# Optimization experiments

Measured on AMD Instinct MI355X. Metric: run time of the kernel, lower is better.

## Reference

```python
import jax, jax.numpy as jnp
import numpy as np

S, D_IN, D = 4, 1024, 256   # n_scales, input dim, d_per_scale (d_model=1024)
B, T = 4, 4096
R_MIN, R_MAX, TH_MIN, TH_MAX = 0.9, 0.999, 0.01, 1.0


def setup_inputs() -> dict:
    key = jax.random.key(0)
    ks = jax.random.split(key, 6)
    s_in = 1.0 / np.sqrt(D_IN)
    s_h = 1.0 / np.sqrt(D)
    return {
        'x':   jax.random.normal(ks[0], (B, T, D_IN), jnp.float32),
        'Wg1': jax.random.normal(ks[1], (S, D_IN, D), jnp.float32) * s_in,
        'bg1': jnp.zeros((S, D), jnp.float32),
        'Wg2': jax.random.normal(ks[2], (S, D, D), jnp.float32) * s_h,
        'bg2': jnp.full((S, D), -4.0, jnp.float32),  # bias_init=constant(-4.0)
        'Wdr': jax.random.normal(ks[3], (S, D_IN, D), jnp.float32) * s_in,
        'bdr': jnp.zeros((S, D), jnp.float32),
        'Wdi': jax.random.normal(ks[4], (S, D_IN, D), jnp.float32) * s_in,
        'bdi': jnp.zeros((S, D), jnp.float32),
    }


def _scale_consts():
    r = np.concatenate([[1.0], np.linspace(R_MAX, R_MIN, S - 1)])
    theta = np.concatenate([[0.0], np.linspace(TH_MIN, TH_MAX, S - 1)])
    a_base = (r * np.exp(1j * theta)).astype(np.complex64)        # (S,)
    bscale = np.where(r >= 1.0, 1.0 / np.sqrt(D), 1.0 - r).astype(np.float32)  # (S,)
    return jnp.asarray(a_base), jnp.asarray(bscale)


def reference(x, Wg1, bg1, Wg2, bg2, Wdr, bdr, Wdi, bdi):
    a_base, bscale = _scale_consts()
    # gate MLP (conditioning = x): (B,S,T,D)
    g1 = jax.nn.relu(jnp.einsum('bti,sid->bstd', x, Wg1) + bg1[None, :, None, :])
    gate = jax.nn.sigmoid(jnp.einsum('bstd,sde->bste', g1, Wg2) + bg2[None, :, None, :])
    # complex drive
    dre = jnp.einsum('bti,sid->bstd', x, Wdr) + bdr[None, :, None, :]
    dim = jnp.einsum('bti,sid->bstd', x, Wdi) + bdi[None, :, None, :]
    omg = (1.0 - gate).astype(jnp.complex64)                       # (B,S,T,D)
    a = omg * a_base[None, :, None, None]
    b = omg * ((dre + 1j * dim).astype(jnp.complex64) * bscale[None, :, None, None])
    # linear recurrence h_t = a_t*h_{t-1} + b_t via associative scan along time
    def binop(left, right):
        al, bl = left
        ar, br = right
        return (al * ar, ar * bl + br)
    _, h = jax.lax.associative_scan(binop, (a, b), axis=2)         # (B,S,T,D)
    h = jnp.moveaxis(h, 1, 2)                                      # (B,T,S,D)
    out = jnp.stack([h.real, h.imag], axis=3)                      # (B,T,S,2,D) -> re/im per scale
    return out.reshape(B, T, S * 2 * D)
```

## Files before the change

### kernel.cpp

```cpp
#include <hip/hip_runtime.h>
#include <cmath>

#define S_   4
#define DIN  1024
#define D_   256
#define B_   4
#define T_   4096
#define BT_  (B_*T_)
#define GN   (S_*3*D_)
#define CHUNKS 128
#define CL   (T_/CHUNKS)

typedef short bf16x8 __attribute__((ext_vector_type(8)));
typedef float f32x4  __attribute__((ext_vector_type(4)));

struct SC { float are[S_]; float aim[S_]; float bsc[S_]; };

__device__ inline unsigned short f2bf(float f) {
    unsigned int u = __builtin_bit_cast(unsigned int, f);
    unsigned int r = (u + 0x7FFFu + ((u >> 16) & 1u)) >> 16;
    return (unsigned short)r;
}
__device__ inline float bf2f_lo(unsigned int u) {
    return __builtin_bit_cast(float, u << 16);
}
__device__ inline float bf2f_hi(unsigned int u) {
    return __builtin_bit_cast(float, u & 0xFFFF0000u);
}
__device__ inline float u16om(unsigned int u) {
    return ((float)u + 0.5f) * (1.f/65536.f);
}

#define GLD_LDS(gp, lp) \
    __builtin_amdgcn_global_load_lds( \
        (const __attribute__((address_space(1))) void*)(gp), \
        (__attribute__((address_space(3))) void*)(lp), 16, 0, 0)

__global__ __launch_bounds__(256) void kconv_x(
    const float* __restrict__ x, unsigned short* __restrict__ xb)
{
    const size_t i = ((size_t)blockIdx.x*256 + threadIdx.x)*4;
    const float4 v = *(const float4*)(x + i);
    ushort4 o;
    o.x = f2bf(v.x); o.y = f2bf(v.y); o.z = f2bf(v.z); o.w = f2bf(v.w);
    *(ushort4*)(xb + i) = o;
}

__global__ __launch_bounds__(256) void kconv_w(
    const float* __restrict__ src, unsigned short* __restrict__ dst,
    int K, int N, size_t dst_s_stride)
{
    __shared__ float t[32][33];
    const int k0 = blockIdx.x*32, n0 = blockIdx.y*32, s = blockIdx.z;
    const float* sp = src + (size_t)s*K*N;
    unsigned short* dp = dst + (size_t)s*dst_s_stride;
    const int c = threadIdx.x & 31, r0 = threadIdx.x >> 5;
    #pragma unroll
    for (int p = 0; p < 4; ++p)
        t[r0 + p*8][c] = sp[(size_t)(k0 + r0 + p*8)*N + n0 + c];
    __syncthreads();
    #pragma unroll
    for (int p = 0; p < 4; ++p)
        dp[(size_t)(n0 + r0 + p*8)*K + k0 + c] = f2bf(t[c][r0 + p*8]);
}

__global__ __launch_bounds__(256) void kconv_w3(
    const float* __restrict__ Wg1, const float* __restrict__ Wdr,
    const float* __restrict__ Wdi, unsigned short* __restrict__ dst)
{
    __shared__ float t[32][33];
    const int z = blockIdx.z;
    const int widx = z >> 2, s = z & 3;
    const float* src = (widx == 0) ? Wg1 : ((widx == 1) ? Wdr : Wdi);
    const float* sp = src + (size_t)s*DIN*D_;
    unsigned short* dp = dst + (size_t)s*768*DIN + (size_t)widx*D_*DIN;
    const int k0 = blockIdx.x*32, n0 = blockIdx.y*32;
    const int c = threadIdx.x & 31, r0 = threadIdx.x >> 5;
    #pragma unroll
    for (int p = 0; p < 4; ++p)
        t[r0 + p*8][c] = sp[(size_t)(k0 + r0 + p*8)*D_ + n0 + c];
    __syncthreads();
    #pragma unroll
    for (int p = 0; p < 4; ++p)
        dp[(size_t)(n0 + r0 + p*8)*DIN + k0 + c] = f2bf(t[c][r0 + p*8]);
}

template<bool DRVB>
__global__ __launch_bounds__(512, 2) void k1_8p(
    const unsigned short* __restrict__ xb,
    const unsigned short* __restrict__ Bct,
    const float* __restrict__ bg1, const float* __restrict__ bdr,
    const float* __restrict__ bdi,
    unsigned short* __restrict__ g1b,
    unsigned short* __restrict__ drvb, float* __restrict__ drvf)
{
    __shared__ unsigned short L[8*8192];

    const int tid  = threadIdx.x;
    const int wave = tid >> 6, lane = tid & 63;
    const int wmr  = wave >> 2;
    const int wnr  = wave & 3;
    const int row0 = blockIdx.x * 256, col0 = blockIdx.y * 256;
    const int cn = lane & 15, quad = lane >> 4;
    const int e8 = cn & 7;
    const int srow = lane >> 3;
    const int lksw = ((lane & 7) ^ srow) * 8;

    const unsigned short* Ag = xb  + (size_t)row0 * DIN;
    const unsigned short* Bg = Bct + (size_t)col0 * DIN;

    f32x4 acc[8][4];
    const f32x4 z = {0.f, 0.f, 0.f, 0.f};
    #pragma unroll
    for (int i = 0; i < 8; ++i)
        #pragma unroll
        for (int j = 0; j < 4; ++j) acc[i][j] = z;

#define SLOT(b,o,h) (L + (((b)*4 + (o)*2 + (h)) * 8192))
#define STAGE(b,o,h,kt,Gp) do { \
    const unsigned short* _g = (Gp) + (size_t)((h)*128 + wave*8 + srow)*DIN \
                             + (size_t)(kt)*64 + lksw; \
    unsigned short* _l = SLOT(b,o,h) + wave*512; \
    GLD_LDS(_g, _l); \
    GLD_LDS(_g + (size_t)64*DIN, _l + 4096); \
} while(0)

#define PHASE(b, ih, jh, STG, WT) do { \
    bf16x8 af[4][2], bfv[2][2]; \
    _Pragma("unroll") \
    for (int ii = 0; ii < 4; ++ii) { \
        const unsigned short* ap = SLOT(b,0,ih) + (size_t)(wmr*64 + ii*16 + cn)*64; \
        _Pragma("unroll") \
        for (int kk = 0; kk < 2; ++kk) \
            af[ii][kk] = *(const bf16x8*)(ap + ((kk*4 + quad) ^ e8)*8); \
    } \
    _Pragma("unroll") \
    for (int jj = 0; jj < 2; ++jj) { \
        const unsigned short* bp = SLOT(b,1,jh) + (size_t)(wnr*32 + jj*16 + cn)*64; \
        _Pragma("unroll") \
        for (int kk = 0; kk < 2; ++kk) \
            bfv[jj][kk] = *(const bf16x8*)(bp + ((kk*4 + quad) ^ e8)*8); \
    } \
    STG; \
    WT; \
    __builtin_amdgcn_s_barrier(); \
    asm volatile("s_waitcnt lgkmcnt(0)" ::: "memory"); \
    __builtin_amdgcn_s_setprio(1); \
    _Pragma("unroll") \
    for (int ii = 0; ii < 4; ++ii) \
        _Pragma("unroll") \
        for (int jj = 0; jj < 2; ++jj) \
            _Pragma("unroll") \
            for (int kk = 0; kk < 2; ++kk) \
                acc[(ih)*4 + ii][(jh)*2 + jj] = \
                    __builtin_amdgcn_mfma_f32_16x16x32_bf16( \
                        af[ii][kk], bfv[jj][kk], \
                        acc[(ih)*4 + ii][(jh)*2 + jj], 0, 0, 0); \
    __builtin_amdgcn_s_setprio(0); \
    __builtin_amdgcn_s_barrier(); \
} while(0)

    STAGE(0,0,0, 0, Ag); STAGE(0,1,0, 0, Bg);
    STAGE(0,0,1, 0, Ag); STAGE(0,1,1, 0, Bg);
    STAGE(1,0,0, 1, Ag); STAGE(1,1,1, 1, Bg);
    asm volatile("s_waitcnt vmcnt(4)" ::: "memory");
    __builtin_amdgcn_s_barrier();

    #pragma unroll 1
    for (int it = 0; it < 8; ++it) {
        const int t1 = 2*it + 1, t2 = 2*it + 2, t3 = 2*it + 3;
        const bool pf = (it < 7);
        PHASE(0, 0, 0, { STAGE(1,0,1, t1, Ag); }, {});
        PHASE(0, 0, 1, { STAGE(1,1,0, t1, Bg); }, {});
        PHASE(0, 1, 1, { if (pf) STAGE(0,0,0, t2, Ag); }, {});
        PHASE(0, 1, 0, { if (pf) STAGE(0,1,1, t2, Bg); },
              { if (pf) asm volatile("s_waitcnt vmcnt(4)" ::: "memory");
                else    asm volatile("s_waitcnt vmcnt(0)" ::: "memory"); });
        PHASE(1, 0, 0, { if (pf) STAGE(0,0,1, t2, Ag); }, {});
        PHASE(1, 0, 1, { if (pf) STAGE(0,1,0, t2, Bg); }, {});
        PHASE(1, 1, 1, { if (pf) STAGE(1,0,0, t3, Ag); }, {});
        PHASE(1, 1, 0, { if (pf) STAGE(1,1,1, t3, Bg); },
              { if (pf) asm volatile("s_waitcnt vmcnt(4)" ::: "memory");
                else    asm volatile("s_waitcnt vmcnt(0)" ::: "memory"); });
    }
#undef PHASE
#undef STAGE
#undef SLOT

    const int s    = col0 / 768;
    const int rem  = col0 - s*768;
    const int mat  = rem >> 8;
    const float* bias = (mat == 0) ? bg1 : ((mat == 1) ? bdr : bdi);

    int dloc[4]; float bv[4];
    #pragma unroll
    for (int j = 0; j < 4; ++j) {
        dloc[j] = (j >> 1)*128 + wnr*32 + (j & 1)*16 + cn;
        bv[j] = bias[s*D_ + dloc[j]];
    }

    #pragma unroll
    for (int i = 0; i < 8; ++i) {
        const int m = row0 + (i >> 2)*128 + wmr*64 + (i & 3)*16 + quad*4;
        #pragma unroll
        for (int j = 0; j < 4; ++j) {
            const int d = dloc[j];
            const f32x4 v = acc[i][j];
            if (mat == 0) {
                unsigned short* gp = g1b + ((size_t)s*BT_ + m)*D_ + d;
                #pragma unroll
                for (int r = 0; r < 4; ++r)
                    gp[(size_t)r*D_] = f2bf(fmaxf(v[r] + bv[j], 0.f));
            } else {
                const size_t base = (size_t)m*(S_*2*D_) + s*2*D_
                                  + (mat == 2 ? D_ : 0) + d;
                if (DRVB) {
                    #pragma unroll
                    for (int r = 0; r < 4; ++r)
                        drvb[base + (size_t)r*(S_*2*D_)] = f2bf(v[r] + bv[j]);
                } else {
                    #pragma unroll
                    for (int r = 0; r < 4; ++r)
                        drvf[base + (size_t)r*(S_*2*D_)] = v[r] + bv[j];
                }
            }
        }
    }
}

__global__ __launch_bounds__(256) void k2_mfma(
    const unsigned short* __restrict__ g1b,
    const unsigned short* __restrict__ B2t,
    const float* __restrict__ bg2, unsigned short* __restrict__ omgu)
{
    __shared__ unsigned short As[128*64];
    __shared__ unsigned short Bs[128*64];

    const int tid = threadIdx.x;
    const int wave = tid >> 6, lane = tid & 63;
    const int wm = (wave >> 1) * 64, wn = (wave & 1) * 64;
    const int row0 = blockIdx.x * 128, col0 = blockIdx.y * 128;
    const int s = blockIdx.z;

    const f32x4 z = {0.f, 0.f, 0.f, 0.f};
    f32x4 acc[4][4];
    #pragma unroll
    for (int i = 0; i < 4; ++i)
        #pragma unroll
        for (int j = 0; j < 4; ++j) acc[i][j] = z;

    const unsigned short* Ag = g1b + ((size_t)s*BT_ + row0)*D_;
    const unsigned short* Bg = B2t + (size_t)s*D_*D_ + (size_t)col0*D_;
    const int lrow = lane >> 3;
    const int lksw = ((lane & 7) ^ lrow) * 8;
    const int cn   = lane & 15, quad = lane >> 4;
    const int e    = cn & 7;

    for (int k0 = 0; k0 < D_; k0 += 64) {
        #pragma unroll
        for (int t = 0; t < 4; ++t) {
            const int m0 = wave*32 + t*8;
            GLD_LDS(Ag + (size_t)(m0 + lrow)*D_ + k0 + lksw, As + m0*64);
            GLD_LDS(Bg + (size_t)(m0 + lrow)*D_ + k0 + lksw, Bs + m0*64);
        }
        __syncthreads();
        #pragma unroll
        for (int ks = 0; ks < 2; ++ks) {
            const int offs = (((ks*4 + quad) ^ e)) * 8;
            bf16x8 af[4], bfv[4];
            #pragma unroll
            for (int i = 0; i < 4; ++i)
                af[i] = *(const bf16x8*)(As + (wm + i*16 + cn)*64 + offs);
            #pragma unroll
            for (int j = 0; j < 4; ++j)
                bfv[j] = *(const bf16x8*)(Bs + (wn + j*16 + cn)*64 + offs);
            #pragma unroll
            for (int i = 0; i < 4; ++i)
                #pragma unroll
                for (int j = 0; j < 4; ++j)
                    acc[i][j] = __builtin_amdgcn_mfma_f32_16x16x32_bf16(
                        af[i], bfv[j], acc[i][j], 0, 0, 0);
        }
        __syncthreads();
    }

    const int qr = quad * 4;
    float bv[4];
    #pragma unroll
    for (int j = 0; j < 4; ++j) bv[j] = bg2[s*D_ + col0 + wn + j*16 + cn];

    #pragma unroll
    for (int i = 0; i < 4; ++i) {
        const int m = row0 + wm + i*16 + qr;
        #pragma unroll
        for (int j = 0; j < 4; ++j) {
            const int d = col0 + wn + j*16 + cn;
            const f32x4 v = acc[i][j];
            unsigned short* op = omgu + ((size_t)s*BT_ + m)*D_ + d;
            #pragma unroll
            for (int r = 0; r < 4; ++r) {
                const float om = 1.f / (1.f + __expf(v[r] + bv[j]));
                op[(size_t)r*D_] =
                    (unsigned short)fminf(om * 65536.f, 65535.f);
            }
        }
    }
}

template<bool DRVB>
__global__ __launch_bounds__(128) void k3a_chunk(
    const unsigned short* __restrict__ omgu,
    const unsigned short* __restrict__ drvb, const float* __restrict__ drvf,
    float4* __restrict__ summ, SC sc)
{
    const int blk = blockIdx.x;
    const int c = blk & (CHUNKS-1);
    const int s = (blk >> 7) & (S_-1);
    const int b = blk >> 9;
    const int d2 = threadIdx.x;

    const float are = sc.are[s], aim = sc.aim[s], bs = sc.bsc[s];
    float Ar[2] = {1.f,1.f}, Ai[2] = {0,0}, Hr[2] = {0,0}, Hi[2] = {0,0};
    const int t0 = c * CL;

    #pragma unroll 4
    for (int t = 0; t < CL; ++t) {
        const int bt = b*T_ + t0 + t;
        const unsigned int ov =
            *(const unsigned int*)(omgu + ((size_t)s*BT_ + bt)*D_ + 2*d2);
        const float om[2] = { u16om(ov & 0xFFFFu), u16om(ov >> 16) };
        const size_t base = (size_t)bt*(S_*2*D_) + s*2*D_ + 2*d2;
        float dre[2], dim[2];
        if (DRVB) {
            const unsigned int ur = *(const unsigned int*)(drvb + base);
            const unsigned int ui = *(const unsigned int*)(drvb + base + D_);
            dre[0] = bf2f_lo(ur); dre[1] = bf2f_hi(ur);
            dim[0] = bf2f_lo(ui); dim[1] = bf2f_hi(ui);
        } else {
            const float2 fr = *(const float2*)(drvf + base);
            const float2 fi = *(const float2*)(drvf + base + D_);
            dre[0] = fr.x; dre[1] = fr.y; dim[0] = fi.x; dim[1] = fi.y;
        }
        #pragma unroll
        for (int u = 0; u < 2; ++u) {
            const float ar = om[u]*are, ai = om[u]*aim, ob = om[u]*bs;
            const float br = ob*dre[u], bi = ob*dim[u];
            const float nHr = ar*Hr[u] - ai*Hi[u] + br;
            const float nHi = ar*Hi[u] + ai*Hr[u] + bi;
            const float nAr = ar*Ar[u] - ai*Ai[u];
            const float nAi = ar*Ai[u] + ai*Ar[u];
            Hr[u]=nHr; Hi[u]=nHi; Ar[u]=nAr; Ai[u]=nAi;
        }
    }
    const size_t so = ((size_t)(b*S_ + s)*CHUNKS + c)*D_ + 2*d2;
    summ[so]     = make_float4(Ar[0], Ai[0], Hr[0], Hi[0]);
    summ[so + 1] = make_float4(Ar[1], Ai[1], Hr[1], Hi[1]);
}

__global__ __launch_bounds__(256) void k3b_scan(float4* __restrict__ summ)
{
    __shared__ float4 sb[2][CHUNKS];
    const int ch = threadIdx.x >> 7;
    const int c  = threadIdx.x & (CHUNKS-1);
    const int channel = blockIdx.x*2 + ch;
    const int d = channel & (D_-1);
    const int s = (channel >> 8) & (S_-1);
    const int b = channel >> 10;
    const size_t off = ((size_t)(b*S_ + s)*CHUNKS + c)*D_ + d;

    float4 v = summ[off];
    sb[ch][c] = v;
    __syncthreads();
    #pragma unroll
    for (int st = 1; st < CHUNKS; st <<= 1) {
        float4 l;
        if (c >= st) l = sb[ch][c - st];
        __syncthreads();
        if (c >= st) {
            float4 nv;
            nv.x = l.x*v.x - l.y*v.y;
            nv.y = l.x*v.y + l.y*v.x;
            nv.z = v.x*l.z - v.y*l.w + v.z;
            nv.w = v.x*l.w + v.y*l.z + v.w;
            v = nv;
            sb[ch][c] = v;
        }
        __syncthreads();
    }
    float2 carry = make_float2(0.f, 0.f);
    if (c > 0) { const float4 p = sb[ch][c-1]; carry = make_float2(p.z, p.w); }
    *(float2*)&summ[off] = carry;
}

template<bool DRVB>
__global__ __launch_bounds__(128) void k3c_final(
    const unsigned short* __restrict__ omgu,
    const unsigned short* __restrict__ drvb, const float* __restrict__ drvf,
    float* __restrict__ out, const float4* __restrict__ summ, SC sc)
{
    const int blk = blockIdx.x;
    const int c = blk & (CHUNKS-1);
    const int s = (blk >> 7) & (S_-1);
    const int b = blk >> 9;
    const int d2 = threadIdx.x;

    const float are = sc.are[s], aim = sc.aim[s], bs = sc.bsc[s];
    const size_t so = ((size_t)(b*S_ + s)*CHUNKS + c)*D_ + 2*d2;
    const float4 v0 = summ[so];
    const float4 v1 = summ[so + 1];
    float Hr[2] = {v0.x, v1.x}, Hi[2] = {v0.y, v1.y};
    const int t0 = c * CL;

    #pragma unroll 4
    for (int t = 0; t < CL; ++t) {
        const int bt = b*T_ + t0 + t;
        const unsigned int ov =
            *(const unsigned int*)(omgu + ((size_t)s*BT_ + bt)*D_ + 2*d2);
        const float om[2] = { u16om(ov & 0xFFFFu), u16om(ov >> 16) };
        const size_t base = (size_t)bt*(S_*2*D_) + s*2*D_ + 2*d2;
        float dre[2], dim[2];
        if (DRVB) {
            const unsigned int ur = *(const unsigned int*)(drvb + base);
            const unsigned int ui = *(const unsigned int*)(drvb + base + D_);
            dre[0] = bf2f_lo(ur); dre[1] = bf2f_hi(ur);
            dim[0] = bf2f_lo(ui); dim[1] = bf2f_hi(ui);
        } else {
            const float2 fr = *(const float2*)(drvf + base);
            const float2 fi = *(const float2*)(drvf + base + D_);
            dre[0] = fr.x; dre[1] = fr.y; dim[0] = fi.x; dim[1] = fi.y;
        }
        #pragma unroll
        for (int u = 0; u < 2; ++u) {
            const float ar = om[u]*are, ai = om[u]*aim, ob = om[u]*bs;
            const float br = ob*dre[u], bi = ob*dim[u];
            const float nHr = ar*Hr[u] - ai*Hi[u] + br;
            const float nHi = ar*Hi[u] + ai*Hr[u] + bi;
            Hr[u]=nHr; Hi[u]=nHi;
        }
        *(float2*)(out + base)      = make_float2(Hr[0], Hr[1]);
        *(float2*)(out + base + D_) = make_float2(Hi[0], Hi[1]);
    }
}

extern "C" void kernel_launch(void* const* d_in, const int* in_sizes, int n_in,
                              void* d_out, int out_size, void* d_ws, size_t ws_size,
                              hipStream_t stream)
{
    const float* x   = (const float*)d_in[0];
    const float* Wg1 = (const float*)d_in[1];
    const float* bg1 = (const float*)d_in[2];
    const float* Wg2 = (const float*)d_in[3];
    const float* bg2 = (const float*)d_in[4];
    const float* Wdr = (const float*)d_in[5];
    const float* bdr = (const float*)d_in[6];
    const float* Wdi = (const float*)d_in[7];
    const float* bdi = (const float*)d_in[8];
    float* out = (float*)d_out;

    char* ws = (char*)d_ws;
    unsigned short* g1b  = (unsigned short*)(ws + 0);
    float4*         summ = (float4*)(ws + 0);
    unsigned short* B2t  = (unsigned short*)(ws + 33554432);
    unsigned short* xb   = (unsigned short*)(ws + 34078720);
    unsigned short* omgu = (unsigned short*)(ws + 34078720);
    unsigned short* Bct  = (unsigned short*)(ws + 67633152);
    unsigned short* drvb = (unsigned short*)(ws + 73924608);
    const bool drv_bf16 = ws_size >= (size_t)73924608 + 67108864;

    SC sc;
    {
        const double r[S_]  = {1.0, 0.999, 0.9495, 0.9};
        const double th[S_] = {0.0, 0.01, 0.505, 1.0};
        for (int s = 0; s < S_; ++s) {
            sc.are[s] = (float)(r[s] * cos(th[s]));
            sc.aim[s] = (float)(r[s] * sin(th[s]));
            sc.bsc[s] = (r[s] >= 1.0) ? (float)(1.0/16.0) : (float)(1.0 - r[s]);
        }
    }

    kconv_x<<<(BT_*DIN)/1024, 256, 0, stream>>>(x, xb);
    kconv_w3<<<dim3(32,8,12), 256, 0, stream>>>(Wg1, Wdr, Wdi, Bct);
    kconv_w<<<dim3(8,8,S_),  256, 0, stream>>>(Wg2, B2t, D_, D_, (size_t)D_*D_);

    if (drv_bf16)
        k1_8p<true><<<dim3(BT_/256, GN/256), 512, 0, stream>>>(
            xb, Bct, bg1, bdr, bdi, g1b, drvb, out);
    else
        k1_8p<false><<<dim3(BT_/256, GN/256), 512, 0, stream>>>(
            xb, Bct, bg1, bdr, bdi, g1b, drvb, out);
    k2_mfma<<<dim3(BT_/128, D_/128, S_), 256, 0, stream>>>(g1b, B2t, bg2, omgu);

    if (drv_bf16) {
        k3a_chunk<true><<<B_*S_*CHUNKS, 128, 0, stream>>>(omgu, drvb, out, summ, sc);
        k3b_scan       <<<(B_*S_*D_)/2, 256, 0, stream>>>(summ);
        k3c_final<true><<<B_*S_*CHUNKS, 128, 0, stream>>>(omgu, drvb, out, out, summ, sc);
    } else {
        k3a_chunk<false><<<B_*S_*CHUNKS, 128, 0, stream>>>(omgu, drvb, out, summ, sc);
        k3b_scan        <<<(B_*S_*D_)/2, 256, 0, stream>>>(summ);
        k3c_final<false><<<B_*S_*CHUNKS, 128, 0, stream>>>(omgu, drvb, out, out, summ, sc);
    }
}
```

Measured before the change: 406.6 us.

## Fuse chunked scan stages into one cooperative kernel with register-cached inputs

Replaces the three-kernel chunked scan (chunk summaries, cross-chunk scan, final pass) with one cooperative kernel that uses grid-wide syncs between phases. Each thread keeps its chunk's omega and bf16 drive values in registers, so the final pass does not re-read them from global memory. This removes two kernel launches and a second read of the inputs, at the cost of two grid barriers, high register pressure from caching 32 timesteps, and an occupancy requirement. The old path is kept as a fallback when occupancy is too low or the cooperative launch fails.

```diff
diff --git a/kernel.cpp b/kernel.cpp
--- a/kernel.cpp
+++ b/kernel.cpp
@@ -1,4 +1,5 @@
 #include <hip/hip_runtime.h>
+#include <hip/hip_cooperative_groups.h>
 #include <cmath>
 
 #define S_   4
@@ -308,6 +309,132 @@
 }
 
 template<bool DRVB>
+__global__ __launch_bounds__(128, 4) void k3_fused(
+    const unsigned short* __restrict__ omgu,
+    const unsigned short* __restrict__ drvb, const float* __restrict__ drvf,
+    float* __restrict__ out, float4* __restrict__ summ, SC sc)
+{
+    __shared__ float4 sb[CHUNKS];
+    const int blk = blockIdx.x;
+    const int c = blk & (CHUNKS-1);
+    const int s = (blk >> 7) & (S_-1);
+    const int b = blk >> 9;
+    const int d2 = threadIdx.x;
+
+    const float are = sc.are[s], aim = sc.aim[s], bs = sc.bsc[s];
+    const int t0 = c * CL;
+
+    unsigned int cO[CL], cR[CL], cI[CL];
+
+    {
+        float Ar[2] = {1.f,1.f}, Ai[2] = {0,0}, Hr[2] = {0,0}, Hi[2] = {0,0};
+        #pragma unroll
+        for (int t = 0; t < CL; ++t) {
+            const int bt = b*T_ + t0 + t;
+            const unsigned int ov =
+                *(const unsigned int*)(omgu + ((size_t)s*BT_ + bt)*D_ + 2*d2);
+            cO[t] = ov;
+            const float om[2] = { u16om(ov & 0xFFFFu), u16om(ov >> 16) };
+            const size_t base = (size_t)bt*(S_*2*D_) + s*2*D_ + 2*d2;
+            float dre[2], dim[2];
+            if (DRVB) {
+                const unsigned int ur = *(const unsigned int*)(drvb + base);
+                const unsigned int ui = *(const unsigned int*)(drvb + base + D_);
+                cR[t] = ur; cI[t] = ui;
+                dre[0] = bf2f_lo(ur); dre[1] = bf2f_hi(ur);
+                dim[0] = bf2f_lo(ui); dim[1] = bf2f_hi(ui);
+            } else {
+                const float2 fr = *(const float2*)(drvf + base);
+                const float2 fi = *(const float2*)(drvf + base + D_);
+                dre[0] = fr.x; dre[1] = fr.y; dim[0] = fi.x; dim[1] = fi.y;
+            }
+            #pragma unroll
+            for (int u = 0; u < 2; ++u) {
+                const float ar = om[u]*are, ai = om[u]*aim, ob = om[u]*bs;
+                const float br = ob*dre[u], bi = ob*dim[u];
+                const float nHr = ar*Hr[u] - ai*Hi[u] + br;
+                const float nHi = ar*Hi[u] + ai*Hr[u] + bi;
+                const float nAr = ar*Ar[u] - ai*Ai[u];
+                const float nAi = ar*Ai[u] + ai*Ar[u];
+                Hr[u]=nHr; Hi[u]=nHi; Ar[u]=nAr; Ai[u]=nAi;
+            }
+        }
+        const size_t so = ((size_t)(b*S_ + s)*CHUNKS + c)*D_ + 2*d2;
+        summ[so]     = make_float4(Ar[0], Ai[0], Hr[0], Hi[0]);
+        summ[so + 1] = make_float4(Ar[1], Ai[1], Hr[1], Hi[1]);
+    }
+
+    cooperative_groups::this_grid().sync();
+
+    #pragma unroll 1
+    for (int ch = 0; ch < 2; ++ch) {
+        const int channel = blk*2 + ch;
+        const int dd = channel & (D_-1);
+        const int ss = (channel >> 8) & (S_-1);
+        const int bb = channel >> 10;
+        const size_t off = ((size_t)(bb*S_ + ss)*CHUNKS + d2)*D_ + dd;
+        float4 v = summ[off];
+        sb[d2] = v;
+        __syncthreads();
+        #pragma unroll 1
+        for (int st = 1; st < CHUNKS; st <<= 1) {
+            float4 l;
+            if (d2 >= st) l = sb[d2 - st];
+            __syncthreads();
+            if (d2 >= st) {
+                float4 nv;
+                nv.x = l.x*v.x - l.y*v.y;
+                nv.y = l.x*v.y + l.y*v.x;
+                nv.z = v.x*l.z - v.y*l.w + v.z;
+                nv.w = v.x*l.w + v.y*l.z + v.w;
+                v = nv;
+                sb[d2] = v;
+            }
+            __syncthreads();
+        }
+        float2 carry = make_float2(0.f, 0.f);
+        if (d2 > 0) { const float4 p = sb[d2-1]; carry = make_float2(p.z, p.w); }
+        *(float2*)&summ[off] = carry;
+        __syncthreads();
+    }
+
+    cooperative_groups::this_grid().sync();
+
+    {
+        const size_t so = ((size_t)(b*S_ + s)*CHUNKS + c)*D_ + 2*d2;
+        const float2 c0 = *(const float2*)&summ[so];
+        const float2 c1 = *(const float2*)&summ[so + 1];
+        float Hr[2] = {c0.x, c1.x}, Hi[2] = {c0.y, c1.y};
+        #pragma unroll
+        for (int t = 0; t < CL; ++t) {
+            const int bt = b*T_ + t0 + t;
+            const unsigned int ov = cO[t];
+            const float om[2] = { u16om(ov & 0xFFFFu), u16om(ov >> 16) };
+            const size_t base = (size_t)bt*(S_*2*D_) + s*2*D_ + 2*d2;
+            float dre[2], dim[2];
+            if (DRVB) {
+                dre[0] = bf2f_lo(cR[t]); dre[1] = bf2f_hi(cR[t]);
+                dim[0] = bf2f_lo(cI[t]); dim[1] = bf2f_hi(cI[t]);
+            } else {
+                const float2 fr = *(const float2*)(drvf + base);
+                const float2 fi = *(const float2*)(drvf + base + D_);
+                dre[0] = fr.x; dre[1] = fr.y; dim[0] = fi.x; dim[1] = fi.y;
+            }
+            #pragma unroll
+            for (int u = 0; u < 2; ++u) {
+                const float ar = om[u]*are, ai = om[u]*aim, ob = om[u]*bs;
+                const float br = ob*dre[u], bi = ob*dim[u];
+                const float nHr = ar*Hr[u] - ai*Hi[u] + br;
+                const float nHi = ar*Hi[u] + ai*Hr[u] + bi;
+                Hr[u]=nHr; Hi[u]=nHi;
+            }
+            *(float2*)(out + base)      = make_float2(Hr[0], Hr[1]);
+            *(float2*)(out + base + D_) = make_float2(Hi[0], Hi[1]);
+        }
+    }
+}
+
+template<bool DRVB>
 __global__ __launch_bounds__(128) void k3a_chunk(
     const unsigned short* __restrict__ omgu,
     const unsigned short* __restrict__ drvb, const float* __restrict__ drvf,
@@ -490,13 +617,40 @@
             xb, Bct, bg1, bdr, bdi, g1b, drvb, out);
     k2_mfma<<<dim3(BT_/128, D_/128, S_), 256, 0, stream>>>(g1b, B2t, bg2, omgu);
 
-    if (drv_bf16) {
-        k3a_chunk<true><<<B_*S_*CHUNKS, 128, 0, stream>>>(omgu, drvb, out, summ, sc);
-        k3b_scan       <<<(B_*S_*D_)/2, 256, 0, stream>>>(summ);
-        k3c_final<true><<<B_*S_*CHUNKS, 128, 0, stream>>>(omgu, drvb, out, out, summ, sc);
-    } else {
-        k3a_chunk<false><<<B_*S_*CHUNKS, 128, 0, stream>>>(omgu, drvb, out, summ, sc);
-        k3b_scan        <<<(B_*S_*D_)/2, 256, 0, stream>>>(summ);
-        k3c_final<false><<<B_*S_*CHUNKS, 128, 0, stream>>>(omgu, drvb, out, out, summ, sc);
-    }
-}
+    int coopOk = 0;
+    {
+        int nb = 0;
+        hipError_t e = hipOccupancyMaxActiveBlocksPerMultiprocessor(
+            &nb,
+            drv_bf16 ? reinterpret_cast<const void*>(&k3_fused<true>)
+                     : reinterpret_cast<const void*>(&k3_fused<false>),
+            128, 0);
+        if (e == hipSuccess && nb >= 8) coopOk = 1;
+    }
+
+    if (coopOk) {
+        const unsigned short* a_omgu = omgu;
+        const unsigned short* a_drvb = drvb;
+        const float* a_drvf = out;
+        float* a_out = out;
+        float4* a_summ = summ;
+        void* args[6] = { (void*)&a_omgu, (void*)&a_drvb, (void*)&a_drvf,
+                          (void*)&a_out, (void*)&a_summ, (void*)&sc };
+        hipError_t e = hipLaunchCooperativeKernel(
+            drv_bf16 ? reinterpret_cast<const void*>(&k3_fused<true>)
+                     : reinterpret_cast<const void*>(&k3_fused<false>),
+            dim3(B_*S_*CHUNKS), dim3(128), args, 0, stream);
+        if (e != hipSuccess) coopOk = 0;
+    }
+    if (!coopOk) {
+        if (drv_bf16) {
+            k3a_chunk<true><<<B_*S_*CHUNKS, 128, 0, stream>>>(omgu, drvb, out, summ, sc);
+            k3b_scan       <<<(B_*S_*D_)/2, 256, 0, stream>>>(summ);
+            k3c_final<true><<<B_*S_*CHUNKS, 128, 0, stream>>>(omgu, drvb, out, out, summ, sc);
+        } else {
+            k3a_chunk<false><<<B_*S_*CHUNKS, 128, 0, stream>>>(omgu, drvb, out, summ, sc);
+            k3b_scan        <<<(B_*S_*D_)/2, 256, 0, stream>>>(summ);
+            k3c_final<false><<<B_*S_*CHUNKS, 128, 0, stream>>>(omgu, drvb, out, out, summ, sc);
+        }
+    }
+}
```

Result: faster. 393.8 us (-3.1%).

## Fuse gate second GEMM into first GEMM epilogue and merge conversion kernels

Applied to the files above, without the earlier changes.

For tiles holding the gate hidden layer, the first GEMM now writes relu(g1) as bf16 into shared memory and runs the second gate GEMM plus sigmoid inside the same block, writing omgu directly. This removes the g1b round trip through global memory and the separate k2 launch. The three weight and input conversion kernels are also merged into one launch. The cost is extra shared memory (a 32 KB B2 buffer), which may lower occupancy, and load imbalance because only one in three column tiles does the extra GEMM.

```diff
diff --git a/kernel.cpp b/kernel.cpp
--- a/kernel.cpp
+++ b/kernel.cpp
@@ -36,65 +36,67 @@
         (const __attribute__((address_space(1))) void*)(gp), \
         (__attribute__((address_space(3))) void*)(lp), 16, 0, 0)
 
-__global__ __launch_bounds__(256) void kconv_x(
-    const float* __restrict__ x, unsigned short* __restrict__ xb)
+__global__ __launch_bounds__(256) void kconv_all(
+    const float* __restrict__ x,
+    const float* __restrict__ Wg1, const float* __restrict__ Wdr,
+    const float* __restrict__ Wdi, const float* __restrict__ Wg2,
+    unsigned short* __restrict__ xb, unsigned short* __restrict__ Bct,
+    unsigned short* __restrict__ B2t)
 {
-    const size_t i = ((size_t)blockIdx.x*256 + threadIdx.x)*4;
-    const float4 v = *(const float4*)(x + i);
-    ushort4 o;
-    o.x = f2bf(v.x); o.y = f2bf(v.y); o.z = f2bf(v.z); o.w = f2bf(v.w);
-    *(ushort4*)(xb + i) = o;
-}
-
-__global__ __launch_bounds__(256) void kconv_w(
-    const float* __restrict__ src, unsigned short* __restrict__ dst,
-    int K, int N, size_t dst_s_stride)
-{
+    const int bid = blockIdx.x;
+    if (bid < 16384) {
+        const size_t i = ((size_t)bid*256 + threadIdx.x)*4;
+        const float4 v = *(const float4*)(x + i);
+        ushort4 o;
+        o.x = f2bf(v.x); o.y = f2bf(v.y); o.z = f2bf(v.z); o.w = f2bf(v.w);
+        *(ushort4*)(xb + i) = o;
+        return;
+    }
     __shared__ float t[32][33];
-    const int k0 = blockIdx.x*32, n0 = blockIdx.y*32, s = blockIdx.z;
-    const float* sp = src + (size_t)s*K*N;
-    unsigned short* dp = dst + (size_t)s*dst_s_stride;
     const int c = threadIdx.x & 31, r0 = threadIdx.x >> 5;
-    #pragma unroll
-    for (int p = 0; p < 4; ++p)
-        t[r0 + p*8][c] = sp[(size_t)(k0 + r0 + p*8)*N + n0 + c];
-    __syncthreads();
-    #pragma unroll
-    for (int p = 0; p < 4; ++p)
-        dp[(size_t)(n0 + r0 + p*8)*K + k0 + c] = f2bf(t[c][r0 + p*8]);
-}
-
-__global__ __launch_bounds__(256) void kconv_w3(
-    const float* __restrict__ Wg1, const float* __restrict__ Wdr,
-    const float* __restrict__ Wdi, unsigned short* __restrict__ dst)
-{
-    __shared__ float t[32][33];
-    const int z = blockIdx.z;
-    const int widx = z >> 2, s = z & 3;
-    const float* src = (widx == 0) ? Wg1 : ((widx == 1) ? Wdr : Wdi);
-    const float* sp = src + (size_t)s*DIN*D_;
-    unsigned short* dp = dst + (size_t)s*768*DIN + (size_t)widx*D_*DIN;
-    const int k0 = blockIdx.x*32, n0 = blockIdx.y*32;
-    const int c = threadIdx.x & 31, r0 = threadIdx.x >> 5;
-    #pragma unroll
-    for (int p = 0; p < 4; ++p)
-        t[r0 + p*8][c] = sp[(size_t)(k0 + r0 + p*8)*D_ + n0 + c];
-    __syncthreads();
-    #pragma unroll
-    for (int p = 0; p < 4; ++p)
-        dp[(size_t)(n0 + r0 + p*8)*DIN + k0 + c] = f2bf(t[c][r0 + p*8]);
+    if (bid < 19456) {
+        const int tt = bid - 16384;
+        const int kb = tt & 31, nb = (tt >> 5) & 7, z = tt >> 8;
+        const int widx = z >> 2, s = z & 3;
+        const float* src = (widx == 0) ? Wg1 : ((widx == 1) ? Wdr : Wdi);
+        const float* sp = src + (size_t)s*DIN*D_;
+        unsigned short* dp = Bct + (size_t)s*768*DIN + (size_t)widx*D_*DIN;
+        const int k0 = kb*32, n0 = nb*32;
+        #pragma unroll
+        for (int p = 0; p < 4; ++p)
+            t[r0 + p*8][c] = sp[(size_t)(k0 + r0 + p*8)*D_ + n0 + c];
+        __syncthreads();
+        #pragma unroll
+        for (int p = 0; p < 4; ++p)
+            dp[(size_t)(n0 + r0 + p*8)*DIN + k0 + c] = f2bf(t[c][r0 + p*8]);
+    } else {
+        const int tt = bid - 19456;
+        const int kb = tt & 7, nb = (tt >> 3) & 7, s = tt >> 6;
+        const float* sp = Wg2 + (size_t)s*D_*D_;
+        unsigned short* dp = B2t + (size_t)s*D_*D_;
+        const int k0 = kb*32, n0 = nb*32;
+        #pragma unroll
+        for (int p = 0; p < 4; ++p)
+            t[r0 + p*8][c] = sp[(size_t)(k0 + r0 + p*8)*D_ + n0 + c];
+        __syncthreads();
+        #pragma unroll
+        for (int p = 0; p < 4; ++p)
+            dp[(size_t)(n0 + r0 + p*8)*D_ + k0 + c] = f2bf(t[c][r0 + p*8]);
+    }
 }
 
 template<bool DRVB>
 __global__ __launch_bounds__(512, 2) void k1_8p(
     const unsigned short* __restrict__ xb,
     const unsigned short* __restrict__ Bct,
-    const float* __restrict__ bg1, const float* __restrict__ bdr,
-    const float* __restrict__ bdi,
-    unsigned short* __restrict__ g1b,
+    const unsigned short* __restrict__ B2t,
+    const float* __restrict__ bg1, const float* __restrict__ bg2,
+    const float* __restrict__ bdr, const float* __restrict__ bdi,
+    unsigned short* __restrict__ omgu,
     unsigned short* __restrict__ drvb, float* __restrict__ drvf)
 {
     __shared__ unsigned short L[8*8192];
+    __shared__ unsigned short Bs2[16384];
 
     const int tid  = threadIdx.x;
     const int wave = tid >> 6, lane = tid & 63;
@@ -190,28 +192,107 @@
     const int s    = col0 / 768;
     const int rem  = col0 - s*768;
     const int mat  = rem >> 8;
-    const float* bias = (mat == 0) ? bg1 : ((mat == 1) ? bdr : bdi);
-
-    int dloc[4]; float bv[4];
-    #pragma unroll
-    for (int j = 0; j < 4; ++j) {
-        dloc[j] = (j >> 1)*128 + wnr*32 + (j & 1)*16 + cn;
-        bv[j] = bias[s*D_ + dloc[j]];
-    }
-
-    #pragma unroll
-    for (int i = 0; i < 8; ++i) {
-        const int m = row0 + (i >> 2)*128 + wmr*64 + (i & 3)*16 + quad*4;
+
+    if (mat == 0) {
+        int dloc[4]; float bv[4];
         #pragma unroll
         for (int j = 0; j < 4; ++j) {
-            const int d = dloc[j];
-            const f32x4 v = acc[i][j];
-            if (mat == 0) {
-                unsigned short* gp = g1b + ((size_t)s*BT_ + m)*D_ + d;
+            dloc[j] = (j >> 1)*128 + wnr*32 + (j & 1)*16 + cn;
+            bv[j] = bg1[s*D_ + dloc[j]];
+        }
+        __syncthreads();
+        #pragma unroll
+        for (int i = 0; i < 8; ++i) {
+            const int rowb = (i >> 2)*128 + wmr*64 + (i & 3)*16 + quad*4;
+            #pragma unroll
+            for (int j = 0; j < 4; ++j) {
+                const int c = dloc[j];
+                const int sl = (c >> 6)*16384, cc = c & 63, c7 = c & 7;
                 #pragma unroll
-                for (int r = 0; r < 4; ++r)
-                    gp[(size_t)r*D_] = f2bf(fmaxf(v[r] + bv[j], 0.f));
-            } else {
+                for (int r = 0; r < 4; ++r) {
+                    const int row = rowb + r;
+                    L[sl + row*64 + (((cc >> 3) ^ (row & 7))*8) + c7] =
+                        f2bf(fmaxf(acc[i][j][r] + bv[j], 0.f));
+                }
+            }
+        }
+        __syncthreads();
+
+        const unsigned short* B2p = B2t + (size_t)s*D_*D_;
+        f32x4 acc2[8][4];
+        #pragma unroll
+        for (int i = 0; i < 8; ++i)
+            #pragma unroll
+            for (int j = 0; j < 4; ++j) acc2[i][j] = z;
+
+        #pragma unroll 1
+        for (int kt = 0; kt < 4; ++kt) {
+            #pragma unroll
+            for (int ld = 0; ld < 4; ++ld)
+                GLD_LDS(B2p + (size_t)(ld*64 + wave*8 + srow)*D_ + kt*64 + lksw,
+                        Bs2 + (ld*64 + wave*8)*64);
+            asm volatile("s_waitcnt vmcnt(0)" ::: "memory");
+            __syncthreads();
+            bf16x8 b2[4][2];
+            #pragma unroll
+            for (int jj = 0; jj < 4; ++jj)
+                #pragma unroll
+                for (int kk = 0; kk < 2; ++kk)
+                    b2[jj][kk] = *(const bf16x8*)(Bs2
+                        + (size_t)(wnr*64 + jj*16 + cn)*64
+                        + ((kk*4 + quad) ^ e8)*8);
+            #pragma unroll
+            for (int ii = 0; ii < 8; ++ii) {
+                bf16x8 a2[2];
+                #pragma unroll
+                for (int kk = 0; kk < 2; ++kk)
+                    a2[kk] = *(const bf16x8*)(L + kt*16384
+                        + (size_t)(wmr*128 + ii*16 + cn)*64
+                        + ((kk*4 + quad) ^ e8)*8);
+                #pragma unroll
+                for (int kk = 0; kk < 2; ++kk)
+                    #pragma unroll
+                    for (int jj = 0; jj < 4; ++jj)
+                        acc2[ii][jj] = __builtin_amdgcn_mfma_f32_16x16x32_bf16(
+                            a2[kk], b2[jj][kk], acc2[ii][jj], 0, 0, 0);
+            }
+            __syncthreads();
+        }
+
+        float bv2[4];
+        #pragma unroll
+        for (int jj = 0; jj < 4; ++jj)
+            bv2[jj] = bg2[s*D_ + wnr*64 + jj*16 + cn];
+        #pragma unroll
+        for (int ii = 0; ii < 8; ++ii) {
+            const int m = row0 + wmr*128 + ii*16 + quad*4;
+            #pragma unroll
+            for (int jj = 0; jj < 4; ++jj) {
+                const int d = wnr*64 + jj*16 + cn;
+                unsigned short* op = omgu + ((size_t)s*BT_ + m)*D_ + d;
+                #pragma unroll
+                for (int r = 0; r < 4; ++r) {
+                    const float om = 1.f / (1.f + __expf(acc2[ii][jj][r] + bv2[jj]));
+                    op[(size_t)r*D_] =
+                        (unsigned short)fminf(om * 65536.f, 65535.f);
+                }
+            }
+        }
+    } else {
+        const float* bias = (mat == 1) ? bdr : bdi;
+        int dloc[4]; float bv[4];
+        #pragma unroll
+        for (int j = 0; j < 4; ++j) {
+            dloc[j] = (j >> 1)*128 + wnr*32 + (j & 1)*16 + cn;
+            bv[j] = bias[s*D_ + dloc[j]];
+        }
+        #pragma unroll
+        for (int i = 0; i < 8; ++i) {
+            const int m = row0 + (i >> 2)*128 + wmr*64 + (i & 3)*16 + quad*4;
+            #pragma unroll
+            for (int j = 0; j < 4; ++j) {
+                const int d = dloc[j];
+                const f32x4 v = acc[i][j];
                 const size_t base = (size_t)m*(S_*2*D_) + s*2*D_
                                   + (mat == 2 ? D_ : 0) + d;
                 if (DRVB) {
@@ -223,85 +304,6 @@
                     for (int r = 0; r < 4; ++r)
                         drvf[base + (size_t)r*(S_*2*D_)] = v[r] + bv[j];
                 }
-            }
-        }
-    }
-}
-
-__global__ __launch_bounds__(256) void k2_mfma(
-    const unsigned short* __restrict__ g1b,
-    const unsigned short* __restrict__ B2t,
-    const float* __restrict__ bg2, unsigned short* __restrict__ omgu)
-{
-    __shared__ unsigned short As[128*64];
-    __shared__ unsigned short Bs[128*64];
-
-    const int tid = threadIdx.x;
-    const int wave = tid >> 6, lane = tid & 63;
-    const int wm = (wave >> 1) * 64, wn = (wave & 1) * 64;
-    const int row0 = blockIdx.x * 128, col0 = blockIdx.y * 128;
-    const int s = blockIdx.z;
-
-    const f32x4 z = {0.f, 0.f, 0.f, 0.f};
-    f32x4 acc[4][4];
-    #pragma unroll
-    for (int i = 0; i < 4; ++i)
-        #pragma unroll
-        for (int j = 0; j < 4; ++j) acc[i][j] = z;
-
-    const unsigned short* Ag = g1b + ((size_t)s*BT_ + row0)*D_;
-    const unsigned short* Bg = B2t + (size_t)s*D_*D_ + (size_t)col0*D_;
-    const int lrow = lane >> 3;
-    const int lksw = ((lane & 7) ^ lrow) * 8;
-    const int cn   = lane & 15, quad = lane >> 4;
-    const int e    = cn & 7;
-
-    for (int k0 = 0; k0 < D_; k0 += 64) {
-        #pragma unroll
-        for (int t = 0; t < 4; ++t) {
-            const int m0 = wave*32 + t*8;
-            GLD_LDS(Ag + (size_t)(m0 + lrow)*D_ + k0 + lksw, As + m0*64);
-            GLD_LDS(Bg + (size_t)(m0 + lrow)*D_ + k0 + lksw, Bs + m0*64);
-        }
-        __syncthreads();
-        #pragma unroll
-        for (int ks = 0; ks < 2; ++ks) {
-            const int offs = (((ks*4 + quad) ^ e)) * 8;
-            bf16x8 af[4], bfv[4];
-            #pragma unroll
-            for (int i = 0; i < 4; ++i)
-                af[i] = *(const bf16x8*)(As + (wm + i*16 + cn)*64 + offs);
-            #pragma unroll
-            for (int j = 0; j < 4; ++j)
-                bfv[j] = *(const bf16x8*)(Bs + (wn + j*16 + cn)*64 + offs);
-            #pragma unroll
-            for (int i = 0; i < 4; ++i)
-                #pragma unroll
-                for (int j = 0; j < 4; ++j)
-                    acc[i][j] = __builtin_amdgcn_mfma_f32_16x16x32_bf16(
-                        af[i], bfv[j], acc[i][j], 0, 0, 0);
-        }
-        __syncthreads();
-    }
-
-    const int qr = quad * 4;
-    float bv[4];
-    #pragma unroll
-    for (int j = 0; j < 4; ++j) bv[j] = bg2[s*D_ + col0 + wn + j*16 + cn];
-
-    #pragma unroll
-    for (int i = 0; i < 4; ++i) {
-        const int m = row0 + wm + i*16 + qr;
-        #pragma unroll
-        for (int j = 0; j < 4; ++j) {
-            const int d = col0 + wn + j*16 + cn;
-            const f32x4 v = acc[i][j];
-            unsigned short* op = omgu + ((size_t)s*BT_ + m)*D_ + d;
-            #pragma unroll
-            for (int r = 0; r < 4; ++r) {
-                const float om = 1.f / (1.f + __expf(v[r] + bv[j]));
-                op[(size_t)r*D_] =
-                    (unsigned short)fminf(om * 65536.f, 65535.f);
             }
         }
     }
@@ -458,11 +460,10 @@
     float* out = (float*)d_out;
 
     char* ws = (char*)d_ws;
-    unsigned short* g1b  = (unsigned short*)(ws + 0);
-    float4*         summ = (float4*)(ws + 0);
+    unsigned short* omgu = (unsigned short*)(ws + 0);
     unsigned short* B2t  = (unsigned short*)(ws + 33554432);
     unsigned short* xb   = (unsigned short*)(ws + 34078720);
-    unsigned short* omgu = (unsigned short*)(ws + 34078720);
+    float4*         summ = (float4*)(ws + 34078720);
     unsigned short* Bct  = (unsigned short*)(ws + 67633152);
     unsigned short* drvb = (unsigned short*)(ws + 73924608);
     const bool drv_bf16 = ws_size >= (size_t)73924608 + 67108864;
@@ -478,17 +479,14 @@
         }
     }
 
-    kconv_x<<<(BT_*DIN)/1024, 256, 0, stream>>>(x, xb);
-    kconv_w3<<<dim3(32,8,12), 256, 0, stream>>>(Wg1, Wdr, Wdi, Bct);
-    kconv_w<<<dim3(8,8,S_),  256, 0, stream>>>(Wg2, B2t, D_, D_, (size_t)D_*D_);
+    kconv_all<<<19712, 256, 0, stream>>>(x, Wg1, Wdr, Wdi, Wg2, xb, Bct, B2t);
 
     if (drv_bf16)
         k1_8p<true><<<dim3(BT_/256, GN/256), 512, 0, stream>>>(
-            xb, Bct, bg1, bdr, bdi, g1b, drvb, out);
+            xb, Bct, B2t, bg1, bg2, bdr, bdi, omgu, drvb, out);
     else
         k1_8p<false><<<dim3(BT_/256, GN/256), 512, 0, stream>>>(
-            xb, Bct, bg1, bdr, bdi, g1b, drvb, out);
-    k2_mfma<<<dim3(BT_/128, D_/128, S_), 256, 0, stream>>>(g1b, B2t, bg2, omgu);
+            xb, Bct, B2t, bg1, bg2, bdr, bdi, omgu, drvb, out);
 
     if (drv_bf16) {
         k3a_chunk<true><<<B_*S_*CHUNKS, 128, 0, stream>>>(omgu, drvb, out, summ, sc);
```

Measured after the change: 411.2 us. No clear change (+1.1%).
